# Performance work log

Measured on AMD Instinct MI355X. Metric: run time of the kernel, lower is better.

The kernel has to match this reference:

```python
import jax, jax.numpy as jnp
import numpy as np


def setup_inputs() -> dict:
    key = jax.random.key(0)
    ks = jax.random.split(key, 5)
    B, S, D, H, dk = 4, 2048, 1024, 16, 64
    s = 0.02
    return {
        "x": jax.random.normal(ks[0], (B, S, D), dtype=jnp.float32),
        "Wq": jax.random.normal(ks[1], (H, D, dk), dtype=jnp.float32) * s,
        "Wk": jax.random.normal(ks[2], (H, D, dk), dtype=jnp.float32) * s,
        "Wv": jax.random.normal(ks[3], (H, D, dk), dtype=jnp.float32) * s,
        "Wo": jax.random.normal(ks[4], (H * dk, D), dtype=jnp.float32) * s,
    }


def reference(x, Wq, Wk, Wv, Wo):
    # Per-head projections: [B,S,D] x [H,D,dk] -> [B,H,S,dk]
    Q = jnp.einsum("bsd,hdk->bhsk", x, Wq)
    K = jnp.einsum("bsd,hdk->bhsk", x, Wk)
    V = jnp.einsum("bsd,hdk->bhsk", x, Wv)
    scale = 1.0 / jnp.sqrt(jnp.asarray(Wq.shape[-1], x.dtype))
    scores = jnp.einsum("bhqk,bhsk->bhqs", Q, K) * scale  # [B,H,S,S]
    attn = jax.nn.softmax(scores, axis=-1)
    out = jnp.einsum("bhqs,bhsk->bhqk", attn, V)  # [B,H,S,dk]
    B, H, S, dk = out.shape
    # concat heads along feature dim (matches torch.cat over head outputs)
    out = out.transpose(0, 2, 1, 3).reshape(B, S, H * dk)
    return out @ Wo  # [B,S,D]
```

## Files before the change

kernel.cpp:

```cpp
#include <hip/hip_runtime.h>
#include <hip/hip_bf16.h>
#include <stdint.h>

typedef __attribute__((ext_vector_type(8))) short bf16x8;
typedef __attribute__((ext_vector_type(4))) float f32x4;
typedef __attribute__((ext_vector_type(4))) unsigned short us4;

#define AS1C(p) ((const __attribute__((address_space(1))) void*)(p))
#define AS3(p)  ((__attribute__((address_space(3))) void*)(p))

#if __has_builtin(__builtin_amdgcn_exp2f)
#define EXP2(x) __builtin_amdgcn_exp2f(x)
#else
#define EXP2(x) __expf((x) * 0.69314718f)
#endif

#define MAX3(a,b,c) fmaxf(fmaxf((a),(b)),(c))

static __device__ __forceinline__ unsigned short f2b(float f) {
  union { __hip_bfloat16 h; unsigned short u; } cv;
  cv.h = __float2bfloat16(f);
  return cv.u;
}

static __device__ __forceinline__ unsigned int cvtpk(float a, float b) {
  unsigned int r;
  asm("v_cvt_pk_bf16_f32 %0, %1, %2" : "=v"(r) : "v"(a), "v"(b));
  return r;
}

__global__ __launch_bounds__(256) void conv_x_kernel(const float* __restrict__ x,
                                                     unsigned short* __restrict__ xb,
                                                     int n4) {
  int i = blockIdx.x * 256 + threadIdx.x;
  if (i >= n4) return;
  float4 v = ((const float4*)x)[i];
  us4 r = { f2b(v.x), f2b(v.y), f2b(v.z), f2b(v.w) };
  *(us4*)&xb[(size_t)i * 4] = r;
}

__global__ __launch_bounds__(256) void conv_wqkv_kernel(const float* __restrict__ Wq,
                                                        const float* __restrict__ Wk,
                                                        const float* __restrict__ Wv,
                                                        unsigned short* __restrict__ WqkvT) {
  int bid = blockIdx.x;
  int which = bid >> 8;
  int h  = (bid >> 4) & 15;
  int dt = bid & 15;
  const float* W = (which == 0) ? Wq : (which == 1 ? Wk : Wv);
  __shared__ float tile[64][65];
  const int t = threadIdx.x;
  const int c  = t & 63;
  const int r0 = t >> 6;
  const float* src = W + (size_t)h * 65536 + (size_t)dt * 64 * 64;
#pragma unroll
  for (int it = 0; it < 16; ++it) {
    int r = r0 + it * 4;
    tile[r][c] = src[r * 64 + c];
  }
  __syncthreads();
  const size_t n0 = (size_t)which * 1024 + h * 64;
  const int d0 = dt * 64;
#pragma unroll
  for (int it = 0; it < 16; ++it) {
    int cc = r0 + it * 4;
    WqkvT[(n0 + cc) * 1024 + d0 + c] = f2b(tile[c][cc]);
  }
}

__global__ __launch_bounds__(256) void conv_wo_kernel(const float* __restrict__ Wo,
                                                      unsigned short* __restrict__ WoT) {
  int kt = blockIdx.x >> 4, nt = blockIdx.x & 15;
  __shared__ float tile[64][65];
  const int t = threadIdx.x;
  const int c  = t & 63;
  const int r0 = t >> 6;
  const float* src = Wo + (size_t)(kt * 64) * 1024 + nt * 64;
#pragma unroll
  for (int it = 0; it < 16; ++it) {
    int r = r0 + it * 4;
    tile[r][c] = src[(size_t)r * 1024 + c];
  }
  __syncthreads();
#pragma unroll
  for (int it = 0; it < 16; ++it) {
    int cc = r0 + it * 4;
    WoT[((size_t)nt * 64 + cc) * 1024 + kt * 64 + c] = f2b(tile[c][cc]);
  }
}

__global__ __launch_bounds__(256) void gemm_qkv_kernel(
    const unsigned short* __restrict__ A,
    const unsigned short* __restrict__ Bt,
    unsigned short* __restrict__ Q,
    unsigned short* __restrict__ Ko,
    unsigned short* __restrict__ Vt) {
  __shared__ __align__(16) unsigned short sA[128 * 32];
  __shared__ __align__(16) unsigned short sB[128 * 32];
  const int tid  = threadIdx.x;
  const int lane = tid & 63;
  const int wid  = tid >> 6;
  const int wr = wid >> 1, wc = wid & 1;
  const int n0 = blockIdx.y * 24 + blockIdx.x;
  const int n1 = (n0 & 7) * 192 + (n0 >> 3);
  const int brow = (n1 / 24) * 128;
  const int bcol = (n1 % 24) * 128;
  const int K = 1024;

  f32x4 acc[4][4] = {};

  const int r4 = tid >> 2;
  const int c8 = (tid & 3) * 8;
  const unsigned short* ga = A  + (size_t)(brow + r4) * K + c8;
  const unsigned short* gb = Bt + (size_t)(bcol + r4) * K + c8;
  unsigned short* lAw = sA + wid * 512;
  unsigned short* lBw = sB + wid * 512;

  for (int kb = 0; kb < K; kb += 32) {
    if (kb) __syncthreads();
    __builtin_amdgcn_global_load_lds(AS1C(ga + kb),            AS3(lAw),        16, 0, 0);
    __builtin_amdgcn_global_load_lds(AS1C(ga + 64 * K + kb),   AS3(lAw + 2048), 16, 0, 0);
    __builtin_amdgcn_global_load_lds(AS1C(gb + kb),            AS3(lBw),        16, 0, 0);
    __builtin_amdgcn_global_load_lds(AS1C(gb + 64 * K + kb),   AS3(lBw + 2048), 16, 0, 0);
    __syncthreads();

    bf16x8 af[4], bfr[4];
#pragma unroll
    for (int mi = 0; mi < 4; ++mi)
      af[mi] = *(const bf16x8*)&sA[(wr * 64 + mi * 16 + (lane & 15)) * 32 + (lane >> 4) * 8];
#pragma unroll
    for (int ni = 0; ni < 4; ++ni)
      bfr[ni] = *(const bf16x8*)&sB[(wc * 64 + ni * 16 + (lane & 15)) * 32 + (lane >> 4) * 8];
#pragma unroll
    for (int mi = 0; mi < 4; ++mi)
#pragma unroll
      for (int ni = 0; ni < 4; ++ni)
        acc[mi][ni] = __builtin_amdgcn_mfma_f32_16x16x32_bf16(af[mi], bfr[ni], acc[mi][ni], 0, 0, 0);
  }

#pragma unroll
  for (int mi = 0; mi < 4; ++mi) {
    int row0 = brow + wr * 64 + mi * 16 + (lane >> 4) * 4;
    int b = row0 >> 11, s0 = row0 & 2047;
#pragma unroll
    for (int ni = 0; ni < 4; ++ni) {
      int col = bcol + wc * 64 + ni * 16 + (lane & 15);
      int which = col >> 10;
      int h  = (col >> 6) & 15;
      int kk = col & 63;
      if (which == 2) {
        us4 pk = { f2b(acc[mi][ni][0]), f2b(acc[mi][ni][1]),
                   f2b(acc[mi][ni][2]), f2b(acc[mi][ni][3]) };
        *(us4*)&Vt[((size_t)(b * 16 + h) * 64 + kk) * 2048 + s0] = pk;
      } else {
        unsigned short* dst = (which == 0) ? Q : Ko;
        float scl = (which == 0) ? 0.18033688f : 1.0f;
#pragma unroll
        for (int j = 0; j < 4; ++j)
          dst[((size_t)(b * 16 + h) * 2048 + (s0 + j)) * 64 + kk] = f2b(acc[mi][ni][j] * scl);
      }
    }
  }
}

__global__ __launch_bounds__(256) void gemm_out_kernel(
    const unsigned short* __restrict__ A,
    const unsigned short* __restrict__ Bt,
    float* __restrict__ out) {
  __shared__ __align__(16) unsigned short sA[128 * 32];
  __shared__ __align__(16) unsigned short sB[128 * 32];
  const int tid  = threadIdx.x;
  const int lane = tid & 63;
  const int wid  = tid >> 6;
  const int wr = wid >> 1, wc = wid & 1;
  const int n0 = blockIdx.y * 8 + blockIdx.x;
  const int n1 = (n0 & 7) * 64 + (n0 >> 3);
  const int brow = (n1 >> 3) * 128;
  const int bcol = (n1 & 7) * 128;
  const int K = 1024;

  f32x4 acc[4][4] = {};

  const int r4 = tid >> 2;
  const int c8 = (tid & 3) * 8;
  const unsigned short* ga = A  + (size_t)(brow + r4) * K + c8;
  const unsigned short* gb = Bt + (size_t)(bcol + r4) * K + c8;
  unsigned short* lAw = sA + wid * 512;
  unsigned short* lBw = sB + wid * 512;

  for (int kb = 0; kb < K; kb += 32) {
    if (kb) __syncthreads();
    __builtin_amdgcn_global_load_lds(AS1C(ga + kb),          AS3(lAw),        16, 0, 0);
    __builtin_amdgcn_global_load_lds(AS1C(ga + 64 * K + kb), AS3(lAw + 2048), 16, 0, 0);
    __builtin_amdgcn_global_load_lds(AS1C(gb + kb),          AS3(lBw),        16, 0, 0);
    __builtin_amdgcn_global_load_lds(AS1C(gb + 64 * K + kb), AS3(lBw + 2048), 16, 0, 0);
    __syncthreads();

    bf16x8 af[4], bfr[4];
#pragma unroll
    for (int mi = 0; mi < 4; ++mi)
      af[mi] = *(const bf16x8*)&sA[(wr * 64 + mi * 16 + (lane & 15)) * 32 + (lane >> 4) * 8];
#pragma unroll
    for (int ni = 0; ni < 4; ++ni)
      bfr[ni] = *(const bf16x8*)&sB[(wc * 64 + ni * 16 + (lane & 15)) * 32 + (lane >> 4) * 8];
#pragma unroll
    for (int mi = 0; mi < 4; ++mi)
#pragma unroll
      for (int ni = 0; ni < 4; ++ni)
        acc[mi][ni] = __builtin_amdgcn_mfma_f32_16x16x32_bf16(af[mi], bfr[ni], acc[mi][ni], 0, 0, 0);
  }

#pragma unroll
  for (int mi = 0; mi < 4; ++mi) {
    int row0 = brow + wr * 64 + mi * 16 + (lane >> 4) * 4;
#pragma unroll
    for (int ni = 0; ni < 4; ++ni) {
      int col = bcol + wc * 64 + ni * 16 + (lane & 15);
#pragma unroll
      for (int j = 0; j < 4; ++j)
        out[(size_t)(row0 + j) * 1024 + col] = acc[mi][ni][j];
    }
  }
}

__global__ __launch_bounds__(512) void attn_kernel(
    const unsigned short* __restrict__ Q,
    const unsigned short* __restrict__ K,
    const unsigned short* __restrict__ Vt,
    unsigned short* __restrict__ O) {
  __shared__ __align__(16) unsigned short sK[2][64 * 64];
  __shared__ __align__(16) unsigned short sVt[2][64 * 64];
  __shared__ __align__(16) unsigned short sP[16][16 * 72];

  const int tid = threadIdx.x, lane = tid & 63, w = tid >> 6;
  const int l15 = lane & 15, hi = lane >> 4;
  const int n = blockIdx.x + (blockIdx.y << 3);
  const int bh = (n & 7) * 8 + (n >> 6);
  const int qx = (n >> 3) & 7;
  const int qb = qx * 256;
  const unsigned short* Qp  = Q  + (size_t)bh * 131072;
  const unsigned short* Kp  = K  + (size_t)bh * 131072;
  const unsigned short* Vtp = Vt + (size_t)bh * 131072;

  bf16x8 qf[2][2];
#pragma unroll
  for (int mi = 0; mi < 2; ++mi) {
    int qrow = qb + w * 32 + mi * 16 + l15;
    qf[mi][0] = *(const bf16x8*)&Qp[(size_t)qrow * 64 + hi * 8];
    qf[mi][1] = *(const bf16x8*)&Qp[(size_t)qrow * 64 + 32 + hi * 8];
  }

  bf16x8 ones;
#pragma unroll
  for (int j = 0; j < 8; ++j) ones[j] = (short)0x3F80;

  f32x4 o[2][4] = {};
  f32x4 lacc[2] = {};
  float m_[2] = { 0.f, 0.f };

  const int lrow = lane >> 3;
  const int uch  = (lane & 7) ^ lrow;
  const unsigned short* kg = Kp  + (size_t)(w * 8 + lrow) * 64   + uch * 8;
  const unsigned short* vg = Vtp + (size_t)(w * 8 + lrow) * 2048 + uch * 8;
  unsigned short* dK0 = &sK[0][w * 512];
  unsigned short* dK1 = &sK[1][w * 512];
  unsigned short* dV0 = &sVt[0][w * 512];
  unsigned short* dV1 = &sVt[1][w * 512];

  const int x7 = l15 & 7;
  const int ck0 = (hi ^ x7) * 8;
  const int ck1 = ((hi + 4) ^ x7) * 8;

  __builtin_amdgcn_global_load_lds(AS1C(kg), AS3(dK0), 16, 0, 0);
  __builtin_amdgcn_global_load_lds(AS1C(vg), AS3(dV0), 16, 0, 0);
  __syncthreads();

  for (int kt = 0; kt < 32; ++kt) {
    const int cur = kt & 1;
    if (kt < 31) {
      kg += 4096; vg += 64;
      __builtin_amdgcn_global_load_lds(AS1C(kg), AS3(cur ? dK0 : dK1), 16, 0, 0);
      __builtin_amdgcn_global_load_lds(AS1C(vg), AS3(cur ? dV0 : dV1), 16, 0, 0);
    }
    const unsigned short* sKc  = &sK[cur][0];
    const unsigned short* sVtc = &sVt[cur][0];

#pragma unroll
    for (int mi = 0; mi < 2; ++mi) {
      const float mneg = -m_[mi];
      f32x4 sc[4] = { { mneg, mneg, mneg, mneg }, { mneg, mneg, mneg, mneg },
                      { mneg, mneg, mneg, mneg }, { mneg, mneg, mneg, mneg } };
      __builtin_amdgcn_s_setprio(1);
#pragma unroll
      for (int ni = 0; ni < 4; ++ni) {
        bf16x8 kf0 = *(const bf16x8*)&sKc[(ni * 16 + l15) * 64 + ck0];
        bf16x8 kf1 = *(const bf16x8*)&sKc[(ni * 16 + l15) * 64 + ck1];
        sc[ni] = __builtin_amdgcn_mfma_f32_16x16x32_bf16(kf0, qf[mi][0], sc[ni], 0, 0, 0);
        sc[ni] = __builtin_amdgcn_mfma_f32_16x16x32_bf16(kf1, qf[mi][1], sc[ni], 0, 0, 0);
      }
      __builtin_amdgcn_s_setprio(0);

      float t0 = MAX3(sc[0][0], sc[0][1], sc[0][2]);
      float t1 = MAX3(sc[0][3], sc[1][0], sc[1][1]);
      float t2 = MAX3(sc[1][2], sc[1][3], sc[2][0]);
      float t3 = MAX3(sc[2][1], sc[2][2], sc[2][3]);
      float t4 = MAX3(sc[3][0], sc[3][1], sc[3][2]);
      float pmax = fmaxf(MAX3(t0, t1, t2), MAX3(t3, t4, sc[3][3]));

      if (!__all(pmax <= 8.0f)) {
        pmax = fmaxf(pmax, __shfl_xor(pmax, 16));
        pmax = fmaxf(pmax, __shfl_xor(pmax, 32));
        float delta = fmaxf(pmax, 0.f);
        float alpha = EXP2(-delta);
#pragma unroll
        for (int j = 0; j < 4; ++j) {
          float dj = __shfl(delta, hi * 4 + j);
          float aj = EXP2(-dj);
          lacc[mi][j] *= aj;
#pragma unroll
          for (int ni = 0; ni < 4; ++ni) o[mi][ni][j] *= aj;
        }
#pragma unroll
        for (int ni = 0; ni < 4; ++ni)
#pragma unroll
          for (int r = 0; r < 4; ++r) sc[ni][r] -= delta;
        m_[mi] += delta;
        (void)alpha;
      }

      f32x4 p4[4];
#pragma unroll
      for (int ni = 0; ni < 4; ++ni)
#pragma unroll
        for (int r = 0; r < 4; ++r)
          p4[ni][r] = EXP2(sc[ni][r]);

      unsigned short* pb = &sP[w * 2 + mi][l15 * 72];
#pragma unroll
      for (int ni = 0; ni < 4; ++ni) {
        uint2 pk = { cvtpk(p4[ni][0], p4[ni][1]), cvtpk(p4[ni][2], p4[ni][3]) };
        *(uint2*)&pb[ni * 16 + hi * 4] = pk;
      }
    }

    bf16x8 pa[2][2];
#pragma unroll
    for (int mi = 0; mi < 2; ++mi) {
      pa[mi][0] = *(const bf16x8*)&sP[w * 2 + mi][l15 * 72 + hi * 8];
      pa[mi][1] = *(const bf16x8*)&sP[w * 2 + mi][l15 * 72 + 32 + hi * 8];
    }
    __builtin_amdgcn_s_setprio(1);
#pragma unroll
    for (int mi = 0; mi < 2; ++mi) {
      lacc[mi] = __builtin_amdgcn_mfma_f32_16x16x32_bf16(pa[mi][0], ones, lacc[mi], 0, 0, 0);
      lacc[mi] = __builtin_amdgcn_mfma_f32_16x16x32_bf16(pa[mi][1], ones, lacc[mi], 0, 0, 0);
    }
#pragma unroll
    for (int ni = 0; ni < 4; ++ni) {
      bf16x8 vf0 = *(const bf16x8*)&sVtc[(ni * 16 + l15) * 64 + ck0];
      bf16x8 vf1 = *(const bf16x8*)&sVtc[(ni * 16 + l15) * 64 + ck1];
#pragma unroll
      for (int mi = 0; mi < 2; ++mi) {
        o[mi][ni] = __builtin_amdgcn_mfma_f32_16x16x32_bf16(pa[mi][0], vf0, o[mi][ni], 0, 0, 0);
        o[mi][ni] = __builtin_amdgcn_mfma_f32_16x16x32_bf16(pa[mi][1], vf1, o[mi][ni], 0, 0, 0);
      }
    }
    __builtin_amdgcn_s_setprio(0);

    __syncthreads();
  }

  const int b = bh >> 4, h = bh & 15;
#pragma unroll
  for (int mi = 0; mi < 2; ++mi) {
#pragma unroll
    for (int j = 0; j < 4; ++j) {
      float inv = 1.0f / lacc[mi][j];
      int row = qb + w * 32 + mi * 16 + hi * 4 + j;
#pragma unroll
      for (int ni = 0; ni < 4; ++ni)
        O[((size_t)b * 2048 + row) * 1024 + h * 64 + ni * 16 + l15] = f2b(o[mi][ni][j] * inv);
    }
  }
}

extern "C" void kernel_launch(void* const* d_in, const int* in_sizes, int n_in,
                              void* d_out, int out_size, void* d_ws, size_t ws_size,
                              hipStream_t stream) {
  const float* x  = (const float*)d_in[0];
  const float* Wq = (const float*)d_in[1];
  const float* Wk = (const float*)d_in[2];
  const float* Wv = (const float*)d_in[3];
  const float* Wo = (const float*)d_in[4];
  float* out = (float*)d_out;

  char* w = (char*)d_ws;
  unsigned short* xb   = (unsigned short*)(w);
  unsigned short* wqkv = (unsigned short*)(w + 16777216);
  unsigned short* wo   = (unsigned short*)(w + 23068672);
  unsigned short* Qb   = (unsigned short*)(w + 25165824);
  unsigned short* Kb   = (unsigned short*)(w + 41943040);
  unsigned short* Vtb  = (unsigned short*)(w + 58720256);
  unsigned short* Ob   = (unsigned short*)(w + 75497472);

  conv_x_kernel<<<8192, 256, 0, stream>>>(x, xb, 2097152);
  conv_wqkv_kernel<<<768, 256, 0, stream>>>(Wq, Wk, Wv, wqkv);
  conv_wo_kernel<<<256, 256, 0, stream>>>(Wo, wo);
  gemm_qkv_kernel<<<dim3(24, 64), 256, 0, stream>>>(xb, wqkv, Qb, Kb, Vtb);
  attn_kernel<<<dim3(8, 64), 512, 0, stream>>>(Qb, Kb, Vtb, Ob);
  gemm_out_kernel<<<dim3(8, 64), 256, 0, stream>>>(Ob, wo, out);
}
```

Baseline: 184.6 us.

## Merge conversion kernels into one launch and use 8-wave GEMM blocks

Folds the x, Wqkv and Wo bf16 conversion kernels into a single launch, with block-index ranges picking the job. This removes two kernel launches and their gaps. Both GEMM kernels now run 512 threads per block: each of the 8 waves computes a 32x64 sub-tile and issues half as many global-to-LDS loads per K step. The aim is more waves in flight to hide latency, at the cost of fewer accumulators per wave and less register-level reuse of the B fragments. A dead exp2 in the attention kernel is also removed.

```diff
diff --git a/kernel.cpp b/kernel.cpp
--- a/kernel.cpp
+++ b/kernel.cpp
@@ -29,67 +29,68 @@
   return r;
 }
 
-__global__ __launch_bounds__(256) void conv_x_kernel(const float* __restrict__ x,
-                                                     unsigned short* __restrict__ xb,
-                                                     int n4) {
-  int i = blockIdx.x * 256 + threadIdx.x;
-  if (i >= n4) return;
-  float4 v = ((const float4*)x)[i];
-  us4 r = { f2b(v.x), f2b(v.y), f2b(v.z), f2b(v.w) };
-  *(us4*)&xb[(size_t)i * 4] = r;
-}
-
-__global__ __launch_bounds__(256) void conv_wqkv_kernel(const float* __restrict__ Wq,
-                                                        const float* __restrict__ Wk,
-                                                        const float* __restrict__ Wv,
-                                                        unsigned short* __restrict__ WqkvT) {
-  int bid = blockIdx.x;
-  int which = bid >> 8;
-  int h  = (bid >> 4) & 15;
-  int dt = bid & 15;
-  const float* W = (which == 0) ? Wq : (which == 1 ? Wk : Wv);
+__global__ __launch_bounds__(256) void conv_all_kernel(
+    const float* __restrict__ x,  unsigned short* __restrict__ xb,
+    const float* __restrict__ Wq, const float* __restrict__ Wk,
+    const float* __restrict__ Wv, unsigned short* __restrict__ WqkvT,
+    const float* __restrict__ Wo, unsigned short* __restrict__ WoT) {
   __shared__ float tile[64][65];
+  const int bid = blockIdx.x;
   const int t = threadIdx.x;
+
+  if (bid < 8192) {
+    int i = bid * 256 + t;
+    float4 v = ((const float4*)x)[i];
+    us4 r = { f2b(v.x), f2b(v.y), f2b(v.z), f2b(v.w) };
+    *(us4*)&xb[(size_t)i * 4] = r;
+    return;
+  }
+
   const int c  = t & 63;
   const int r0 = t >> 6;
-  const float* src = W + (size_t)h * 65536 + (size_t)dt * 64 * 64;
-#pragma unroll
-  for (int it = 0; it < 16; ++it) {
-    int r = r0 + it * 4;
-    tile[r][c] = src[r * 64 + c];
-  }
-  __syncthreads();
-  const size_t n0 = (size_t)which * 1024 + h * 64;
-  const int d0 = dt * 64;
-#pragma unroll
-  for (int it = 0; it < 16; ++it) {
-    int cc = r0 + it * 4;
-    WqkvT[(n0 + cc) * 1024 + d0 + c] = f2b(tile[c][cc]);
-  }
-}
-
-__global__ __launch_bounds__(256) void conv_wo_kernel(const float* __restrict__ Wo,
-                                                      unsigned short* __restrict__ WoT) {
-  int kt = blockIdx.x >> 4, nt = blockIdx.x & 15;
-  __shared__ float tile[64][65];
-  const int t = threadIdx.x;
-  const int c  = t & 63;
-  const int r0 = t >> 6;
-  const float* src = Wo + (size_t)(kt * 64) * 1024 + nt * 64;
-#pragma unroll
-  for (int it = 0; it < 16; ++it) {
-    int r = r0 + it * 4;
-    tile[r][c] = src[(size_t)r * 1024 + c];
-  }
-  __syncthreads();
-#pragma unroll
-  for (int it = 0; it < 16; ++it) {
-    int cc = r0 + it * 4;
-    WoT[((size_t)nt * 64 + cc) * 1024 + kt * 64 + c] = f2b(tile[c][cc]);
-  }
-}
-
-__global__ __launch_bounds__(256) void gemm_qkv_kernel(
+
+  if (bid < 8960) {
+    int b2 = bid - 8192;
+    int which = b2 >> 8;
+    int h  = (b2 >> 4) & 15;
+    int dt = b2 & 15;
+    const float* W = (which == 0) ? Wq : (which == 1 ? Wk : Wv);
+    const float* src = W + (size_t)h * 65536 + (size_t)dt * 64 * 64;
+#pragma unroll
+    for (int it = 0; it < 16; ++it) {
+      int r = r0 + it * 4;
+      tile[r][c] = src[r * 64 + c];
+    }
+    __syncthreads();
+    const size_t n0 = (size_t)which * 1024 + h * 64;
+    const int d0 = dt * 64;
+#pragma unroll
+    for (int it = 0; it < 16; ++it) {
+      int cc = r0 + it * 4;
+      WqkvT[(n0 + cc) * 1024 + d0 + c] = f2b(tile[c][cc]);
+    }
+    return;
+  }
+
+  {
+    int b2 = bid - 8960;
+    int kt = b2 >> 4, nt = b2 & 15;
+    const float* src = Wo + (size_t)(kt * 64) * 1024 + nt * 64;
+#pragma unroll
+    for (int it = 0; it < 16; ++it) {
+      int r = r0 + it * 4;
+      tile[r][c] = src[(size_t)r * 1024 + c];
+    }
+    __syncthreads();
+#pragma unroll
+    for (int it = 0; it < 16; ++it) {
+      int cc = r0 + it * 4;
+      WoT[((size_t)nt * 64 + cc) * 1024 + kt * 64 + c] = f2b(tile[c][cc]);
+    }
+  }
+}
+
+__global__ __launch_bounds__(512) void gemm_qkv_kernel(
     const unsigned short* __restrict__ A,
     const unsigned short* __restrict__ Bt,
     unsigned short* __restrict__ Q,
@@ -100,6 +101,7 @@
   const int tid  = threadIdx.x;
   const int lane = tid & 63;
   const int wid  = tid >> 6;
+  const int l15 = lane & 15, hi = lane >> 4;
   const int wr = wid >> 1, wc = wid & 1;
   const int n0 = blockIdx.y * 24 + blockIdx.x;
   const int n1 = (n0 & 7) * 192 + (n0 >> 3);
@@ -107,7 +109,7 @@
   const int bcol = (n1 % 24) * 128;
   const int K = 1024;
 
-  f32x4 acc[4][4] = {};
+  f32x4 acc[2][4] = {};
 
   const int r4 = tid >> 2;
   const int c8 = (tid & 3) * 8;
@@ -118,33 +120,31 @@
 
   for (int kb = 0; kb < K; kb += 32) {
     if (kb) __syncthreads();
-    __builtin_amdgcn_global_load_lds(AS1C(ga + kb),            AS3(lAw),        16, 0, 0);
-    __builtin_amdgcn_global_load_lds(AS1C(ga + 64 * K + kb),   AS3(lAw + 2048), 16, 0, 0);
-    __builtin_amdgcn_global_load_lds(AS1C(gb + kb),            AS3(lBw),        16, 0, 0);
-    __builtin_amdgcn_global_load_lds(AS1C(gb + 64 * K + kb),   AS3(lBw + 2048), 16, 0, 0);
+    __builtin_amdgcn_global_load_lds(AS1C(ga + kb), AS3(lAw), 16, 0, 0);
+    __builtin_amdgcn_global_load_lds(AS1C(gb + kb), AS3(lBw), 16, 0, 0);
     __syncthreads();
 
-    bf16x8 af[4], bfr[4];
-#pragma unroll
-    for (int mi = 0; mi < 4; ++mi)
-      af[mi] = *(const bf16x8*)&sA[(wr * 64 + mi * 16 + (lane & 15)) * 32 + (lane >> 4) * 8];
+    bf16x8 af[2], bfr[4];
+#pragma unroll
+    for (int mi = 0; mi < 2; ++mi)
+      af[mi] = *(const bf16x8*)&sA[(wr * 32 + mi * 16 + l15) * 32 + hi * 8];
 #pragma unroll
     for (int ni = 0; ni < 4; ++ni)
-      bfr[ni] = *(const bf16x8*)&sB[(wc * 64 + ni * 16 + (lane & 15)) * 32 + (lane >> 4) * 8];
-#pragma unroll
-    for (int mi = 0; mi < 4; ++mi)
+      bfr[ni] = *(const bf16x8*)&sB[(wc * 64 + ni * 16 + l15) * 32 + hi * 8];
+#pragma unroll
+    for (int mi = 0; mi < 2; ++mi)
 #pragma unroll
       for (int ni = 0; ni < 4; ++ni)
         acc[mi][ni] = __builtin_amdgcn_mfma_f32_16x16x32_bf16(af[mi], bfr[ni], acc[mi][ni], 0, 0, 0);
   }
 
 #pragma unroll
-  for (int mi = 0; mi < 4; ++mi) {
-    int row0 = brow + wr * 64 + mi * 16 + (lane >> 4) * 4;
+  for (int mi = 0; mi < 2; ++mi) {
+    int row0 = brow + wr * 32 + mi * 16 + hi * 4;
     int b = row0 >> 11, s0 = row0 & 2047;
 #pragma unroll
     for (int ni = 0; ni < 4; ++ni) {
-      int col = bcol + wc * 64 + ni * 16 + (lane & 15);
+      int col = bcol + wc * 64 + ni * 16 + l15;
       int which = col >> 10;
       int h  = (col >> 6) & 15;
       int kk = col & 63;
@@ -163,7 +163,7 @@
   }
 }
 
-__global__ __launch_bounds__(256) void gemm_out_kernel(
+__global__ __launch_bounds__(512) void gemm_out_kernel(
     const unsigned short* __restrict__ A,
     const unsigned short* __restrict__ Bt,
     float* __restrict__ out) {
@@ -172,6 +172,7 @@
   const int tid  = threadIdx.x;
   const int lane = tid & 63;
   const int wid  = tid >> 6;
+  const int l15 = lane & 15, hi = lane >> 4;
   const int wr = wid >> 1, wc = wid & 1;
   const int n0 = blockIdx.y * 8 + blockIdx.x;
   const int n1 = (n0 & 7) * 64 + (n0 >> 3);
@@ -179,7 +180,7 @@
   const int bcol = (n1 & 7) * 128;
   const int K = 1024;
 
-  f32x4 acc[4][4] = {};
+  f32x4 acc[2][4] = {};
 
   const int r4 = tid >> 2;
   const int c8 = (tid & 3) * 8;
@@ -190,32 +191,30 @@
 
   for (int kb = 0; kb < K; kb += 32) {
     if (kb) __syncthreads();
-    __builtin_amdgcn_global_load_lds(AS1C(ga + kb),          AS3(lAw),        16, 0, 0);
-    __builtin_amdgcn_global_load_lds(AS1C(ga + 64 * K + kb), AS3(lAw + 2048), 16, 0, 0);
-    __builtin_amdgcn_global_load_lds(AS1C(gb + kb),          AS3(lBw),        16, 0, 0);
-    __builtin_amdgcn_global_load_lds(AS1C(gb + 64 * K + kb), AS3(lBw + 2048), 16, 0, 0);
+    __builtin_amdgcn_global_load_lds(AS1C(ga + kb), AS3(lAw), 16, 0, 0);
+    __builtin_amdgcn_global_load_lds(AS1C(gb + kb), AS3(lBw), 16, 0, 0);
     __syncthreads();
 
-    bf16x8 af[4], bfr[4];
-#pragma unroll
-    for (int mi = 0; mi < 4; ++mi)
-      af[mi] = *(const bf16x8*)&sA[(wr * 64 + mi * 16 + (lane & 15)) * 32 + (lane >> 4) * 8];
+    bf16x8 af[2], bfr[4];
+#pragma unroll
+    for (int mi = 0; mi < 2; ++mi)
+      af[mi] = *(const bf16x8*)&sA[(wr * 32 + mi * 16 + l15) * 32 + hi * 8];
 #pragma unroll
     for (int ni = 0; ni < 4; ++ni)
-      bfr[ni] = *(const bf16x8*)&sB[(wc * 64 + ni * 16 + (lane & 15)) * 32 + (lane >> 4) * 8];
-#pragma unroll
-    for (int mi = 0; mi < 4; ++mi)
+      bfr[ni] = *(const bf16x8*)&sB[(wc * 64 + ni * 16 + l15) * 32 + hi * 8];
+#pragma unroll
+    for (int mi = 0; mi < 2; ++mi)
 #pragma unroll
       for (int ni = 0; ni < 4; ++ni)
         acc[mi][ni] = __builtin_amdgcn_mfma_f32_16x16x32_bf16(af[mi], bfr[ni], acc[mi][ni], 0, 0, 0);
   }
 
 #pragma unroll
-  for (int mi = 0; mi < 4; ++mi) {
-    int row0 = brow + wr * 64 + mi * 16 + (lane >> 4) * 4;
+  for (int mi = 0; mi < 2; ++mi) {
+    int row0 = brow + wr * 32 + mi * 16 + hi * 4;
 #pragma unroll
     for (int ni = 0; ni < 4; ++ni) {
-      int col = bcol + wc * 64 + ni * 16 + (lane & 15);
+      int col = bcol + wc * 64 + ni * 16 + l15;
 #pragma unroll
       for (int j = 0; j < 4; ++j)
         out[(size_t)(row0 + j) * 1024 + col] = acc[mi][ni][j];
@@ -311,7 +310,6 @@
         pmax = fmaxf(pmax, __shfl_xor(pmax, 16));
         pmax = fmaxf(pmax, __shfl_xor(pmax, 32));
         float delta = fmaxf(pmax, 0.f);
-        float alpha = EXP2(-delta);
 #pragma unroll
         for (int j = 0; j < 4; ++j) {
           float dj = __shfl(delta, hi * 4 + j);
@@ -325,7 +323,6 @@
 #pragma unroll
           for (int r = 0; r < 4; ++r) sc[ni][r] -= delta;
         m_[mi] += delta;
-        (void)alpha;
       }
 
       f32x4 p4[4];
@@ -403,10 +400,8 @@
   unsigned short* Vtb  = (unsigned short*)(w + 58720256);
   unsigned short* Ob   = (unsigned short*)(w + 75497472);
 
-  conv_x_kernel<<<8192, 256, 0, stream>>>(x, xb, 2097152);
-  conv_wqkv_kernel<<<768, 256, 0, stream>>>(Wq, Wk, Wv, wqkv);
-  conv_wo_kernel<<<256, 256, 0, stream>>>(Wo, wo);
-  gemm_qkv_kernel<<<dim3(24, 64), 256, 0, stream>>>(xb, wqkv, Qb, Kb, Vtb);
+  conv_all_kernel<<<9216, 256, 0, stream>>>(x, xb, Wq, Wk, Wv, wqkv, Wo, wo);
+  gemm_qkv_kernel<<<dim3(24, 64), 512, 0, stream>>>(xb, wqkv, Qb, Kb, Vtb);
   attn_kernel<<<dim3(8, 64), 512, 0, stream>>>(Qb, Kb, Vtb, Ob);
-  gemm_out_kernel<<<dim3(8, 64), 256, 0, stream>>>(Ob, wo, out);
-}
+  gemm_out_kernel<<<dim3(8, 64), 512, 0, stream>>>(Ob, wo, out);
+}
```

New measurement: 182.2 us. Within noise of the previous version (-1.3%).
